# Optimization experiments

Measured on AMD Instinct MI355X. Metric: run time of the kernel, lower is better.

Reference implementation:

```python
import jax, jax.numpy as jnp
import numpy as np

B, L, S, H, E, D = 2, 2048, 2048, 16, 64, 64

def setup_inputs() -> dict:
    key = jax.random.key(0)
    kq, kk, kv = jax.random.split(key, 3)
    queries = jax.random.normal(kq, (B, L, H, E), dtype=jnp.float32)
    keys = jax.random.normal(kk, (B, S, H, E), dtype=jnp.float32)
    values = jax.random.normal(kv, (B, S, H, D), dtype=jnp.float32)
    mask = jnp.zeros((1, 1, L, S), dtype=jnp.float32)  # additive mask, broadcast over B,H
    return {"queries": queries, "keys": keys, "values": values, "mask": mask}

def reference(queries, keys, values, mask):
    # scale defaults to 1/sqrt(E)
    scale = 1.0 / jnp.sqrt(jnp.asarray(queries.shape[-1], queries.dtype))
    # scores: [B,H,L,S]
    scores = jnp.einsum('blhe,bshe->bhls', queries, keys)
    scores = scores + mask
    A = jax.nn.softmax(scale * scores, axis=-1)  # dropout rate 0 => identity
    V = jnp.einsum('bhls,bshd->blhd', A, values)
    return V
```

## Files before the change

### kernel.cpp

```cpp
#include <hip/hip_runtime.h>

typedef _Float16 half8 __attribute__((ext_vector_type(8)));
typedef _Float16 half4 __attribute__((ext_vector_type(4)));
typedef float f32x4 __attribute__((ext_vector_type(4)));

constexpr int B = 2, L = 2048, S = 2048, H = 16, E = 64, D = 64;
constexpr int BM = 64;
constexpr int BN = 64;
constexpr int LDT = 72;
constexpr int NTI = S / BN;

__global__ __launch_bounds__(256, 4)
void fa_kernel(const float* __restrict__ Qg, const float* __restrict__ Kg,
               const float* __restrict__ Vg, const float* __restrict__ Mg,
               float* __restrict__ Og)
{
    __shared__ _Float16 sK[BN][LDT];
    __shared__ _Float16 sV[D][LDT];
    __shared__ _Float16 sP[4][16][LDT];

    const int tid  = threadIdx.x;
    const int wave = tid >> 6;
    const int lane = tid & 63;
    const int quad = lane >> 4;
    const int lq   = lane & 15;

    const int i  = blockIdx.x;
    const int bh = (i & 7) * 4 + ((i >> 3) & 3);
    const int qb = i >> 5;
    const int b  = bh >> 4;
    const int h  = bh & 15;
    const int q0 = qb * BM;

    const int rowStride = H * E;
    const size_t qbase = ((size_t)b * L) * rowStride + h * E;
    const size_t kbase = ((size_t)b * S) * rowStride + h * E;

    const float cS = 0.125f * 1.44269504089f;

    half8 qf[2];
    {
        const float* qp = Qg + qbase + (size_t)(q0 + wave*16 + lq) * rowStride + quad*8;
        #pragma unroll
        for (int ks = 0; ks < 2; ++ks)
            #pragma unroll
            for (int j = 0; j < 8; ++j)
                qf[ks][j] = (_Float16)(qp[ks*32 + j] * cS);
    }

    const float* mrow = Mg + (size_t)(q0 + wave*16 + lq) * S;

    float lsum = 0.f;
    f32x4 oacc[4];
    #pragma unroll
    for (int dt = 0; dt < 4; ++dt) oacc[dt] = (f32x4){0.f, 0.f, 0.f, 0.f};

    const int db = tid & 15;
    const int sb = tid >> 4;
    const float* vbase = Vg + kbase + (size_t)(sb*4) * rowStride + db*4;

    for (int t = 0; t < NTI; ++t) {
        const int s0 = t * BN;
        #pragma unroll
        for (int ii = 0; ii < 4; ++ii) {
            int idx = ii*256 + tid;
            int r = idx >> 4, c = (idx & 15)*4;
            const float4 kv = *(const float4*)(Kg + kbase + (size_t)(s0 + r) * rowStride + c);
            half4 hk = {(_Float16)kv.x, (_Float16)kv.y, (_Float16)kv.z, (_Float16)kv.w};
            *(half4*)&sK[r][c] = hk;
        }
        {
            float4 vr[4];
            #pragma unroll
            for (int j = 0; j < 4; ++j)
                vr[j] = *(const float4*)(vbase + (size_t)(s0 + j) * rowStride);
            const int off = (((sb >> 1) ^ (db >> 1)) << 3) + ((sb & 1) << 2);
            #pragma unroll
            for (int j = 0; j < 4; ++j) {
                half4 hv = { (_Float16)((&vr[0].x)[j]), (_Float16)((&vr[1].x)[j]),
                             (_Float16)((&vr[2].x)[j]), (_Float16)((&vr[3].x)[j]) };
                *(half4*)&sV[db*4 + j][off] = hv;
            }
        }
        __syncthreads();

        float4 mv[4];
        #pragma unroll
        for (int nt = 0; nt < 4; ++nt)
            mv[nt] = *(const float4*)(mrow + s0 + nt*16 + quad*4);

        f32x4 sf[4];
        #pragma unroll
        for (int nt = 0; nt < 4; ++nt) {
            half8 kf0 = *(const half8*)&sK[nt*16 + lq][ 0 + quad*8];
            half8 kf1 = *(const half8*)&sK[nt*16 + lq][32 + quad*8];
            f32x4 acc = (f32x4){0.f, 0.f, 0.f, 0.f};
            acc = __builtin_amdgcn_mfma_f32_16x16x32_f16(kf0, qf[0], acc, 0, 0, 0);
            acc = __builtin_amdgcn_mfma_f32_16x16x32_f16(kf1, qf[1], acc, 0, 0, 0);
            sf[nt] = acc;
        }

        #pragma unroll
        for (int nt = 0; nt < 4; ++nt) {
            half4 hp;
            #pragma unroll
            for (int r = 0; r < 4; ++r) {
                float lg = fmaf((&mv[nt].x)[r], cS, sf[nt][r]);
                float p  = __builtin_amdgcn_exp2f(lg);
                lsum += p;
                hp[r] = (_Float16)p;
            }
            *(half4*)&sP[wave][lq][nt*16 + quad*4] = hp;
        }

        #pragma unroll
        for (int ks = 0; ks < 2; ++ks) {
            half8 pf = *(const half8*)&sP[wave][lq][ks*32 + quad*8];
            #pragma unroll
            for (int dt = 0; dt < 4; ++dt) {
                const int vrow = dt*16 + lq;
                const int phys = (ks*4 + quad) ^ ((vrow >> 3) & 7);
                half8 vf = *(const half8*)&sV[vrow][phys << 3];
                oacc[dt] = __builtin_amdgcn_mfma_f32_16x16x32_f16(pf, vf, oacc[dt], 0, 0, 0);
            }
        }
        __syncthreads();
    }

    lsum += __shfl_xor(lsum, 16);
    lsum += __shfl_xor(lsum, 32);

    #pragma unroll
    for (int r = 0; r < 4; ++r) {
        float l_bc = __shfl(lsum, quad*4 + r, 16);
        float inv = 1.f / l_bc;
        float* orow = Og + qbase + (size_t)(q0 + wave*16 + quad*4 + r) * rowStride;
        #pragma unroll
        for (int dt = 0; dt < 4; ++dt)
            orow[dt*16 + lq] = oacc[dt][r] * inv;
    }
}

extern "C" void kernel_launch(void* const* d_in, const int* in_sizes, int n_in,
                              void* d_out, int out_size, void* d_ws, size_t ws_size,
                              hipStream_t stream) {
    const float* Qg = (const float*)d_in[0];
    const float* Kg = (const float*)d_in[1];
    const float* Vg = (const float*)d_in[2];
    const float* Mg = (const float*)d_in[3];
    float* Og = (float*)d_out;
    dim3 grid((L / BM) * B * H);
    fa_kernel<<<grid, 256, 0, stream>>>(Qg, Kg, Vg, Mg, Og);
}
```

Baseline: 195.9 us.

## Prefetch next K/V/mask tile into registers to overlap global loads with compute

Restructures the main loop as a register-staged software pipeline. Global loads of the next K, V and mask tile are issued before the current tile's MFMA and softmax work, then converted to fp16 and written to shared memory after a barrier at the end of the iteration. The intent is to hide global memory latency behind compute. It also raises wave priority around the MFMA blocks with s_setprio; the extra prefetch registers risk pressure under the 4-blocks-per-SM launch bound.

```diff
diff --git a/kernel.cpp b/kernel.cpp
--- a/kernel.cpp
+++ b/kernel.cpp
@@ -58,38 +58,48 @@
     const int db = tid & 15;
     const int sb = tid >> 4;
     const float* vbase = Vg + kbase + (size_t)(sb*4) * rowStride + db*4;
+    const float* krow  = Kg + kbase + (size_t)(tid >> 4) * rowStride + (tid & 15)*4;
+    const int voff = (((sb >> 1) ^ (db >> 1)) << 3) + ((sb & 1) << 2);
+
+    float4 kreg[4], vreg[4], mreg[4];
+
+    #pragma unroll
+    for (int ii = 0; ii < 4; ++ii)
+        kreg[ii] = *(const float4*)(krow + (size_t)(ii*16) * rowStride);
+    #pragma unroll
+    for (int j = 0; j < 4; ++j)
+        vreg[j] = *(const float4*)(vbase + (size_t)j * rowStride);
+    #pragma unroll
+    for (int nt = 0; nt < 4; ++nt)
+        mreg[nt] = *(const float4*)(mrow + nt*16 + quad*4);
+
+    #pragma unroll
+    for (int ii = 0; ii < 4; ++ii) {
+        half4 hk = {(_Float16)kreg[ii].x, (_Float16)kreg[ii].y,
+                    (_Float16)kreg[ii].z, (_Float16)kreg[ii].w};
+        *(half4*)&sK[(tid >> 4) + ii*16][(tid & 15)*4] = hk;
+    }
+    #pragma unroll
+    for (int j = 0; j < 4; ++j) {
+        half4 hv = { (_Float16)((&vreg[0].x)[j]), (_Float16)((&vreg[1].x)[j]),
+                     (_Float16)((&vreg[2].x)[j]), (_Float16)((&vreg[3].x)[j]) };
+        *(half4*)&sV[db*4 + j][voff] = hv;
+    }
+    __syncthreads();
 
     for (int t = 0; t < NTI; ++t) {
-        const int s0 = t * BN;
-        #pragma unroll
-        for (int ii = 0; ii < 4; ++ii) {
-            int idx = ii*256 + tid;
-            int r = idx >> 4, c = (idx & 15)*4;
-            const float4 kv = *(const float4*)(Kg + kbase + (size_t)(s0 + r) * rowStride + c);
-            half4 hk = {(_Float16)kv.x, (_Float16)kv.y, (_Float16)kv.z, (_Float16)kv.w};
-            *(half4*)&sK[r][c] = hk;
-        }
-        {
-            float4 vr[4];
+        if (t + 1 < NTI) {
+            const int s1 = (t + 1) * BN;
+            #pragma unroll
+            for (int ii = 0; ii < 4; ++ii)
+                kreg[ii] = *(const float4*)(krow + (size_t)(s1 + ii*16) * rowStride);
             #pragma unroll
             for (int j = 0; j < 4; ++j)
-                vr[j] = *(const float4*)(vbase + (size_t)(s0 + j) * rowStride);
-            const int off = (((sb >> 1) ^ (db >> 1)) << 3) + ((sb & 1) << 2);
-            #pragma unroll
-            for (int j = 0; j < 4; ++j) {
-                half4 hv = { (_Float16)((&vr[0].x)[j]), (_Float16)((&vr[1].x)[j]),
-                             (_Float16)((&vr[2].x)[j]), (_Float16)((&vr[3].x)[j]) };
-                *(half4*)&sV[db*4 + j][off] = hv;
-            }
+                vreg[j] = *(const float4*)(vbase + (size_t)(s1 + j) * rowStride);
         }
-        __syncthreads();
-
-        float4 mv[4];
-        #pragma unroll
-        for (int nt = 0; nt < 4; ++nt)
-            mv[nt] = *(const float4*)(mrow + s0 + nt*16 + quad*4);
 
         f32x4 sf[4];
+        __builtin_amdgcn_s_setprio(1);
         #pragma unroll
         for (int nt = 0; nt < 4; ++nt) {
             half8 kf0 = *(const half8*)&sK[nt*16 + lq][ 0 + quad*8];
@@ -99,13 +109,14 @@
             acc = __builtin_amdgcn_mfma_f32_16x16x32_f16(kf1, qf[1], acc, 0, 0, 0);
             sf[nt] = acc;
         }
+        __builtin_amdgcn_s_setprio(0);
 
         #pragma unroll
         for (int nt = 0; nt < 4; ++nt) {
             half4 hp;
             #pragma unroll
             for (int r = 0; r < 4; ++r) {
-                float lg = fmaf((&mv[nt].x)[r], cS, sf[nt][r]);
+                float lg = fmaf((&mreg[nt].x)[r], cS, sf[nt][r]);
                 float p  = __builtin_amdgcn_exp2f(lg);
                 lsum += p;
                 hp[r] = (_Float16)p;
@@ -113,6 +124,14 @@
             *(half4*)&sP[wave][lq][nt*16 + quad*4] = hp;
         }
 
+        if (t + 1 < NTI) {
+            const int s1 = (t + 1) * BN;
+            #pragma unroll
+            for (int nt = 0; nt < 4; ++nt)
+                mreg[nt] = *(const float4*)(mrow + s1 + nt*16 + quad*4);
+        }
+
+        __builtin_amdgcn_s_setprio(1);
         #pragma unroll
         for (int ks = 0; ks < 2; ++ks) {
             half8 pf = *(const half8*)&sP[wave][lq][ks*32 + quad*8];
@@ -124,7 +143,24 @@
                 oacc[dt] = __builtin_amdgcn_mfma_f32_16x16x32_f16(pf, vf, oacc[dt], 0, 0, 0);
             }
         }
-        __syncthreads();
+        __builtin_amdgcn_s_setprio(0);
+
+        if (t + 1 < NTI) {
+            __syncthreads();
+            #pragma unroll
+            for (int ii = 0; ii < 4; ++ii) {
+                half4 hk = {(_Float16)kreg[ii].x, (_Float16)kreg[ii].y,
+                            (_Float16)kreg[ii].z, (_Float16)kreg[ii].w};
+                *(half4*)&sK[(tid >> 4) + ii*16][(tid & 15)*4] = hk;
+            }
+            #pragma unroll
+            for (int j = 0; j < 4; ++j) {
+                half4 hv = { (_Float16)((&vreg[0].x)[j]), (_Float16)((&vreg[1].x)[j]),
+                             (_Float16)((&vreg[2].x)[j]), (_Float16)((&vreg[3].x)[j]) };
+                *(half4*)&sV[db*4 + j][voff] = hv;
+            }
+            __syncthreads();
+        }
     }
 
     lsum += __shfl_xor(lsum, 16);
```

Result: no change. 197.1 us (+0.6%).
